# Kernel optimization log

Hardware: AMD Instinct MI355X
Metric: run time of the kernel (lower is better)

Reference implementation:

```python
import jax, jax.numpy as jnp
import numpy as np

MARGIN = 1.0
SIZE_AVERAGE = True


def setup_inputs() -> dict:
    key = jax.random.key(0)
    k1, k2 = jax.random.split(key)
    N, C = 16384, 5000
    score = jax.random.normal(k1, (N, C), dtype=jnp.float32)
    target = jax.random.randint(k2, (N,), 0, C, dtype=jnp.int64)
    return {"score": score, "target": target}


def reference(score, target):
    # score: [N, C], target: [N] int
    N, C = score.shape
    correct = jnp.take_along_axis(score, target[:, None], axis=1)  # [N, 1]
    hinge = jnp.maximum(0.0, MARGIN + score - correct)             # [N, C]
    mask = jnp.arange(C)[None, :] != target[:, None]               # exclude c == target
    loss = jnp.sum(jnp.where(mask, hinge, 0.0))
    cnt = N * (C - 1)
    return loss / cnt if SIZE_AVERAGE else loss
```

## Files before the change

### kernel.cpp

```cpp
#include <hip/hip_runtime.h>

#define MARGIN 1.0f
#define NBLOCKS 2048

__global__ __launch_bounds__(256) void mcl_hinge(const float* __restrict__ score,
                                                 const int* __restrict__ target,
                                                 double* __restrict__ partial,
                                                 int N, int C) {
    float acc = 0.0f;
    const int nvec = C >> 2;

    for (int row = blockIdx.x; row < N; row += gridDim.x) {
        const size_t base = (size_t)row * (size_t)C;
        const float b = MARGIN - score[base + target[row]];
        const float4* __restrict__ rp = reinterpret_cast<const float4*>(score + base);
        for (int i = threadIdx.x; i < nvec; i += 256) {
            float4 v = rp[i];
            acc += fmaxf(0.0f, v.x + b);
            acc += fmaxf(0.0f, v.y + b);
            acc += fmaxf(0.0f, v.z + b);
            acc += fmaxf(0.0f, v.w + b);
        }
        for (int i = (nvec << 2) + (int)threadIdx.x; i < C; i += 256)
            acc += fmaxf(0.0f, score[base + i] + b);
    }

    #pragma unroll
    for (int off = 32; off > 0; off >>= 1)
        acc += __shfl_down(acc, off, 64);

    __shared__ float warp_s[4];
    const int lane = threadIdx.x & 63;
    const int wid  = threadIdx.x >> 6;
    if (lane == 0) warp_s[wid] = acc;
    __syncthreads();
    if (threadIdx.x == 0)
        partial[blockIdx.x] = (double)(warp_s[0] + warp_s[1] + warp_s[2] + warp_s[3]);
}

__global__ __launch_bounds__(256) void mcl_final(const double* __restrict__ partial,
                                                 float* __restrict__ out,
                                                 int NB, int N, int C) {
    double s = 0.0;
    for (int i = threadIdx.x; i < NB; i += 256) s += partial[i];

    #pragma unroll
    for (int off = 32; off > 0; off >>= 1)
        s += __shfl_down(s, off, 64);

    __shared__ double warp_s[4];
    const int lane = threadIdx.x & 63;
    const int wid  = threadIdx.x >> 6;
    if (lane == 0) warp_s[wid] = s;
    __syncthreads();
    if (threadIdx.x == 0) {
        double tot = warp_s[0] + warp_s[1] + warp_s[2] + warp_s[3];
        tot -= (double)N * (double)MARGIN;
        out[0] = (float)(tot / ((double)N * (double)(C - 1)));
    }
}

extern "C" void kernel_launch(void* const* d_in, const int* in_sizes, int n_in,
                              void* d_out, int out_size, void* d_ws, size_t ws_size,
                              hipStream_t stream) {
    const float* score  = (const float*)d_in[0];
    const int*   target = (const int*)d_in[1];
    float* out = (float*)d_out;
    double* ws = (double*)d_ws;

    const int N = in_sizes[1];
    const int C = in_sizes[0] / N;

    mcl_hinge<<<NBLOCKS, 256, 0, stream>>>(score, target, ws, N, C);
    mcl_final<<<1, 256, 0, stream>>>(ws, out, NBLOCKS, N, C);
}
```

Before: 59.18 us.

## Flatten eight-row tiles into one contiguous float4 stream with compile-time width

Adds a kernel specialised for C=5000 in which each block handles 8 consecutive rows as a single flat float4 range, so no lanes sit idle at row tails. The per-row bias values are preloaded into shared memory and looked up by dividing the index by a constant. Trip counts are fixed at compile time and the sum is split across two accumulators. The grid becomes N/8 blocks, and the general kernel is kept as a fallback for other shapes.

```diff
diff --git a/kernel.cpp b/kernel.cpp
--- a/kernel.cpp
+++ b/kernel.cpp
@@ -1,38 +1,80 @@
 #include <hip/hip_runtime.h>
 
 #define MARGIN 1.0f
-#define NBLOCKS 2048
+#define NT 256
+#define ROWS_PER_BLOCK 8
 
-__global__ __launch_bounds__(256) void mcl_hinge(const float* __restrict__ score,
-                                                 const int* __restrict__ target,
-                                                 double* __restrict__ partial,
-                                                 int N, int C) {
-    float acc = 0.0f;
-    const int nvec = C >> 2;
+template <int CC>
+__global__ __launch_bounds__(NT) void mcl_hinge_flat(const float* __restrict__ score,
+                                                     const int* __restrict__ target,
+                                                     double* __restrict__ partial) {
+    constexpr int NV  = CC / 4;
+    constexpr int TOT = ROWS_PER_BLOCK * NV;
+    constexpr int KFULL = (TOT - (NT - 1) + NT - 1) / NT;
+    constexpr int TAIL  = TOT - KFULL * NT;
 
-    for (int row = blockIdx.x; row < N; row += gridDim.x) {
-        const size_t base = (size_t)row * (size_t)C;
-        const float b = MARGIN - score[base + target[row]];
-        const float4* __restrict__ rp = reinterpret_cast<const float4*>(score + base);
-        for (int i = threadIdx.x; i < nvec; i += 256) {
-            float4 v = rp[i];
-            acc += fmaxf(0.0f, v.x + b);
-            acc += fmaxf(0.0f, v.y + b);
-            acc += fmaxf(0.0f, v.z + b);
-            acc += fmaxf(0.0f, v.w + b);
-        }
-        for (int i = (nvec << 2) + (int)threadIdx.x; i < C; i += 256)
-            acc += fmaxf(0.0f, score[base + i] + b);
+    __shared__ float lb[ROWS_PER_BLOCK];
+    const int r0 = blockIdx.x * ROWS_PER_BLOCK;
+    if (threadIdx.x < ROWS_PER_BLOCK) {
+        const int r = r0 + threadIdx.x;
+        lb[threadIdx.x] = MARGIN - score[(size_t)r * CC + target[r]];
     }
+    __syncthreads();
+
+    const float4* __restrict__ rp =
+        reinterpret_cast<const float4*>(score) + (size_t)blockIdx.x * TOT;
+
+    float acc0 = 0.0f, acc1 = 0.0f;
+    int f = threadIdx.x;
+    #pragma unroll 3
+    for (int k = 0; k < KFULL; ++k, f += NT) {
+        const float b = lb[f / NV];
+        const float4 v = rp[f];
+        acc0 += fmaxf(0.0f, v.x + b) + fmaxf(0.0f, v.y + b);
+        acc1 += fmaxf(0.0f, v.z + b) + fmaxf(0.0f, v.w + b);
+    }
+    if (TAIL > 0 && threadIdx.x < TAIL) {
+        const float b = lb[f / NV];
+        const float4 v = rp[f];
+        acc0 += fmaxf(0.0f, v.x + b) + fmaxf(0.0f, v.y + b);
+        acc1 += fmaxf(0.0f, v.z + b) + fmaxf(0.0f, v.w + b);
+    }
+    float acc = acc0 + acc1;
 
     #pragma unroll
     for (int off = 32; off > 0; off >>= 1)
         acc += __shfl_down(acc, off, 64);
 
-    __shared__ float warp_s[4];
-    const int lane = threadIdx.x & 63;
-    const int wid  = threadIdx.x >> 6;
-    if (lane == 0) warp_s[wid] = acc;
+    __shared__ float warp_s[NT / 64];
+    if ((threadIdx.x & 63) == 0) warp_s[threadIdx.x >> 6] = acc;
+    __syncthreads();
+    if (threadIdx.x == 0)
+        partial[blockIdx.x] = (double)(warp_s[0] + warp_s[1] + warp_s[2] + warp_s[3]);
+}
+
+__global__ __launch_bounds__(NT) void mcl_hinge_gen(const float* __restrict__ score,
+                                                    const int* __restrict__ target,
+                                                    double* __restrict__ partial,
+                                                    int N, int C) {
+    float acc = 0.0f;
+    const int nvec = C >> 2;
+    for (int row = blockIdx.x; row < N; row += gridDim.x) {
+        const size_t base = (size_t)row * (size_t)C;
+        const float b = MARGIN - score[base + target[row]];
+        const float4* __restrict__ rp = reinterpret_cast<const float4*>(score + base);
+        for (int i = threadIdx.x; i < nvec; i += NT) {
+            float4 v = rp[i];
+            acc += fmaxf(0.0f, v.x + b) + fmaxf(0.0f, v.y + b)
+                 + fmaxf(0.0f, v.z + b) + fmaxf(0.0f, v.w + b);
+        }
+        for (int i = (nvec << 2) + (int)threadIdx.x; i < C; i += NT)
+            acc += fmaxf(0.0f, score[base + i] + b);
+    }
+    #pragma unroll
+    for (int off = 32; off > 0; off >>= 1)
+        acc += __shfl_down(acc, off, 64);
+    __shared__ float warp_s[NT / 64];
+    if ((threadIdx.x & 63) == 0) warp_s[threadIdx.x >> 6] = acc;
     __syncthreads();
     if (threadIdx.x == 0)
         partial[blockIdx.x] = (double)(warp_s[0] + warp_s[1] + warp_s[2] + warp_s[3]);
@@ -43,15 +85,11 @@
                                                  int NB, int N, int C) {
     double s = 0.0;
     for (int i = threadIdx.x; i < NB; i += 256) s += partial[i];
-
     #pragma unroll
     for (int off = 32; off > 0; off >>= 1)
         s += __shfl_down(s, off, 64);
-
     __shared__ double warp_s[4];
-    const int lane = threadIdx.x & 63;
-    const int wid  = threadIdx.x >> 6;
-    if (lane == 0) warp_s[wid] = s;
+    if ((threadIdx.x & 63) == 0) warp_s[threadIdx.x >> 6] = s;
     __syncthreads();
     if (threadIdx.x == 0) {
         double tot = warp_s[0] + warp_s[1] + warp_s[2] + warp_s[3];
@@ -71,6 +109,13 @@
     const int N = in_sizes[1];
     const int C = in_sizes[0] / N;
 
-    mcl_hinge<<<NBLOCKS, 256, 0, stream>>>(score, target, ws, N, C);
-    mcl_final<<<1, 256, 0, stream>>>(ws, out, NBLOCKS, N, C);
+    if (C == 5000 && (N % ROWS_PER_BLOCK) == 0) {
+        const int nb = N / ROWS_PER_BLOCK;
+        mcl_hinge_flat<5000><<<nb, NT, 0, stream>>>(score, target, ws);
+        mcl_final<<<1, 256, 0, stream>>>(ws, out, nb, N, C);
+    } else {
+        const int nb = 2048;
+        mcl_hinge_gen<<<nb, NT, 0, stream>>>(score, target, ws, N, C);
+        mcl_final<<<1, 256, 0, stream>>>(ws, out, nb, N, C);
+    }
 }
```

Result: no change. 58.65 us (median of 2 runs) (-0.9%).
